# Kernel tuning notes

Hardware: AMD Instinct MI355X
Metric: run time of the kernel (lower is better)

The kernel has to match this reference:

```python
import jax, jax.numpy as jnp
import numpy as np

N, C, H, W = 4, 256, 64, 64
D = 128  # inter_channels = C // 2


def setup_inputs() -> dict:
    key = jax.random.key(0)
    ks = jax.random.split(key, 9)
    s = 0.05  # weight scale
    return {
        "x": jax.random.normal(ks[0], (N, C, H, W), jnp.float32),
        "Wg": jax.random.normal(ks[1], (D, C), jnp.float32) * s,
        "bg": jax.random.normal(ks[2], (D,), jnp.float32) * s,
        "Wt": jax.random.normal(ks[3], (D, C), jnp.float32) * s,
        "bt": jax.random.normal(ks[4], (D,), jnp.float32) * s,
        "Wp": jax.random.normal(ks[5], (D, C), jnp.float32) * s,
        "bp": jax.random.normal(ks[6], (D,), jnp.float32) * s,
        "Wz": jax.random.normal(ks[7], (C, D), jnp.float32) * s,
        "bz": jax.random.normal(ks[8], (C,), jnp.float32) * s,
    }


def reference(x, Wg, bg, Wt, bt, Wp, bp, Wz, bz):
    # NonLocalBlock, mode='embedded', dimension=2, bn_layer=False.
    # 1x1 convs are per-pixel linear maps over channels.
    n, c, h, w = x.shape
    xf = x.reshape(n, c, h * w)                                  # (N,C,S)
    g_x = jnp.einsum('dc,ncs->nds', Wg, xf) + bg[None, :, None]  # (N,D,S)
    th = jnp.einsum('dc,ncs->nds', Wt, xf) + bt[None, :, None]   # (N,D,S)
    ph = jnp.einsum('dc,ncs->nds', Wp, xf) + bp[None, :, None]   # (N,D,S)
    f = jnp.einsum('nds,ndt->nst', th, ph)                       # (N,S,S)
    att = jax.nn.softmax(f, axis=-1)
    y = jnp.einsum('nst,ndt->nds', att, g_x)                     # (N,D,S)
    w_y = jnp.einsum('cd,nds->ncs', Wz, y) + bz[None, :, None]   # (N,C,S)
    return (w_y + xf).reshape(n, c, h, w)
```

## Files before the change

### kernel.cpp

```cpp
#include <hip/hip_runtime.h>
#include <math.h>

#define N_ 4
#define C_ 256
#define D_ 128
#define S_ 4096
#define LOG2E 1.4426950408889634f
#define SPLIT 4
#define TPS 16

typedef __attribute__((ext_vector_type(4))) float f32x4;
typedef __attribute__((ext_vector_type(16))) float f32x16;
typedef __attribute__((ext_vector_type(8))) short short8;
typedef __attribute__((ext_vector_type(8))) unsigned short ushort8;
typedef __attribute__((ext_vector_type(4))) unsigned short ushort4v;

#define MFMA16(a, b, c) __builtin_amdgcn_mfma_f32_16x16x32_bf16((a), (b), (c), 0, 0, 0)
#define MFMA32(a, b, c) __builtin_amdgcn_mfma_f32_32x32x16_bf16((a), (b), (c), 0, 0, 0)

__device__ __forceinline__ unsigned short f2bf(float f) {
  union { float f; unsigned int u; } v; v.f = f;
  unsigned int r = v.u + 0x7fffu + ((v.u >> 16) & 1u);
  return (unsigned short)(r >> 16);
}
__device__ __forceinline__ float bf2f(unsigned short u) {
  union { unsigned int u; float f; } v; v.u = ((unsigned int)u) << 16;
  return v.f;
}
__device__ __forceinline__ unsigned cvtpk(float lo, float hi) {
  unsigned r;
  asm("v_cvt_pk_bf16_f32 %0, %1, %2" : "=v"(r) : "v"(lo), "v"(hi));
  return r;
}
__device__ __forceinline__ float vmax16(const f32x16& v) {
  float a = fmaxf(fmaxf(v[0], v[1]), fmaxf(v[2], v[3]));
  float b = fmaxf(fmaxf(v[4], v[5]), fmaxf(v[6], v[7]));
  float c = fmaxf(fmaxf(v[8], v[9]), fmaxf(v[10], v[11]));
  float d = fmaxf(fmaxf(v[12], v[13]), fmaxf(v[14], v[15]));
  return fmaxf(fmaxf(a, b), fmaxf(c, d));
}
__device__ __forceinline__ float vsum16(const f32x16& v) {
  float a = (v[0] + v[1]) + (v[2] + v[3]);
  float b = (v[4] + v[5]) + (v[6] + v[7]);
  float c = (v[8] + v[9]) + (v[10] + v[11]);
  float d = (v[12] + v[13]) + (v[14] + v[15]);
  return (a + b) + (c + d);
}
__device__ __forceinline__ void gload16(const void* g, void* l) {
  __builtin_amdgcn_global_load_lds((const __attribute__((address_space(1))) unsigned int*)g,
                                   (__attribute__((address_space(3))) unsigned int*)l,
                                   16, 0, 0);
}

__global__ void k_convw(const float* __restrict__ w0, const float* __restrict__ w1,
                        const float* __restrict__ w2, const float* __restrict__ w3,
                        unsigned short* __restrict__ d0, unsigned short* __restrict__ d1,
                        unsigned short* __restrict__ d2, unsigned short* __restrict__ d3) {
  int b = blockIdx.x;
  int w = b >> 4;
  int i = (b & 15) * 256 + threadIdx.x;
  const float* s = (w == 0) ? w0 : (w == 1) ? w1 : (w == 2) ? w2 : w3;
  unsigned short* d = (w == 0) ? d0 : (w == 1) ? d1 : (w == 2) ? d2 : d3;
  const float4* sp = reinterpret_cast<const float4*>(s) + (size_t)i * 2;
  float4 a = sp[0], c = sp[1];
  ushort8 o;
  o[0] = f2bf(a.x); o[1] = f2bf(a.y); o[2] = f2bf(a.z); o[3] = f2bf(a.w);
  o[4] = f2bf(c.x); o[5] = f2bf(c.y); o[6] = f2bf(c.z); o[7] = f2bf(c.w);
  reinterpret_cast<ushort8*>(d)[i] = o;
}

__global__ __launch_bounds__(256, 3) void k_proj(
    const float* __restrict__ x,
    const unsigned short* __restrict__ wg, const unsigned short* __restrict__ wt,
    const unsigned short* __restrict__ wp,
    const float* __restrict__ bg, const float* __restrict__ bt, const float* __restrict__ bp,
    unsigned short* __restrict__ qb, unsigned short* __restrict__ kb, unsigned short* __restrict__ vb)
{
  __shared__ __align__(16) unsigned short xs[C_ * 64];
  const int tid = threadIdx.x;
  const int p = blockIdx.x >> 8;
  const int n = (blockIdx.x >> 6) & 3;
  const int s0 = (blockIdx.x & 63) << 6;
  const float* xsrc = x + (size_t)n * C_ * S_ + s0;
#pragma unroll
  for (int i = 0; i < 16; ++i) {
    int ch = i * 256 + tid;
    int c = ch >> 4, s4 = (ch & 15) << 2;
    float4 v = *reinterpret_cast<const float4*>(xsrc + (size_t)c * S_ + s4);
    ushort4v o;
    o[0] = f2bf(v.x); o[1] = f2bf(v.y); o[2] = f2bf(v.z); o[3] = f2bf(v.w);
    *reinterpret_cast<ushort4v*>(xs + c * 64 + s4) = o;
  }
  __syncthreads();
  const int lane = tid & 63, wid = tid >> 6;
  const int l15 = lane & 15, g = lane >> 4;
  const int scol = wid * 16 + l15;

  short8 bx[8];
#pragma unroll
  for (int kc = 0; kc < 8; ++kc) {
    int cb = kc * 32 + g * 8;
    short8 t;
#pragma unroll
    for (int j = 0; j < 8; ++j) t[j] = (short)xs[(cb + j) * 64 + scol];
    bx[kc] = t;
  }

  const unsigned short* W = (p == 0) ? wg : ((p == 1) ? wt : wp);
  const float* bias = (p == 0) ? bg : ((p == 1) ? bt : bp);
  const f32x4 fz = {0.f, 0.f, 0.f, 0.f};
  f32x4 acc[8];
#pragma unroll
  for (int dt = 0; dt < 8; ++dt) acc[dt] = fz;
#pragma unroll
  for (int dt = 0; dt < 8; ++dt) {
    const unsigned short* wrow = W + (size_t)(dt * 16 + l15) * C_ + g * 8;
#pragma unroll
    for (int kc = 0; kc < 8; ++kc) {
      short8 a = *reinterpret_cast<const short8*>(wrow + kc * 32);
      acc[dt] = MFMA16(a, bx[kc], acc[dt]);
    }
  }
  if (p == 0) {
#pragma unroll
    for (int dt = 0; dt < 8; ++dt) {
#pragma unroll
      for (int r = 0; r < 4; ++r) {
        int d = dt * 16 + 4 * g + r;
        vb[((size_t)n * D_ + d) * S_ + s0 + scol] = f2bf(acc[dt][r] + bias[d]);
      }
    }
  } else {
    unsigned short* dst = (p == 1) ? qb : kb;
    unsigned short* row = dst + ((size_t)(n * S_) + s0 + scol) * D_;
#pragma unroll
    for (int dt = 0; dt < 8; ++dt) {
      ushort4v o;
#pragma unroll
      for (int r = 0; r < 4; ++r) o[r] = f2bf(acc[dt][r] + bias[dt * 16 + 4 * g + r]);
      *reinterpret_cast<ushort4v*>(row + dt * 16 + 4 * g) = o;
    }
  }
}

__global__ __launch_bounds__(512, 2) void k_attn(
    const unsigned short* __restrict__ qb, const unsigned short* __restrict__ kb,
    const unsigned short* __restrict__ vb,
    unsigned short* __restrict__ opart, float2* __restrict__ ml)
{
  __shared__ __align__(16) unsigned short ksm[2][64 * 128];
  __shared__ __align__(16) unsigned short vsm[2][128 * 64];
  const int tid = threadIdx.x, lane = tid & 63, w = tid >> 6;
  const int l31 = lane & 31, hi = lane >> 5;
  const int b = blockIdx.x;
  const int sp = b & 3, qt = (b >> 2) & 15, n = b >> 6;
  const int q0 = qt << 8;

  unsigned koff[2], voff[2], ubo[2];
#pragma unroll
  for (int j = 0; j < 2; ++j) {
    int f = j * 512 + tid;
    int kr = f >> 4, kc = f & 15;
    koff[j] = kr * D_ + ((kc ^ (kr & 7)) << 3);
    int vr = f >> 3, vc = f & 7;
    voff[j] = vr * S_ + ((vc ^ (vr & 7)) << 3);
    ubo[j] = (unsigned)(j * 512 + (tid & 448)) * 8;
  }
  const unsigned short* kb0 = kb + ((size_t)n * S_ + (size_t)sp * TPS * 64) * D_;
  const unsigned short* vb0 = vb + (size_t)n * D_ * S_ + sp * TPS * 64;

  auto stage = [&](int buf, int t) {
    const unsigned short* kt = kb0 + (size_t)t * 64 * D_;
    const unsigned short* vt = vb0 + t * 64;
#pragma unroll
    for (int j = 0; j < 2; ++j) gload16(kt + koff[j], &ksm[buf][ubo[j]]);
#pragma unroll
    for (int j = 0; j < 2; ++j) gload16(vt + voff[j], &vsm[buf][ubo[j]]);
  };

  stage(0, 0);

  const unsigned short* qsrc = qb + ((size_t)(n * S_) + q0 + w * 32 + l31) * D_;
  short8 qf[8];
#pragma unroll
  for (int k = 0; k < 8; ++k)
    qf[k] = *reinterpret_cast<const short8*>(qsrc + k * 16 + hi * 8);

  const f32x16 z16 = {0.f,0.f,0.f,0.f,0.f,0.f,0.f,0.f,0.f,0.f,0.f,0.f,0.f,0.f,0.f,0.f};
  f32x16 oacc[4];
#pragma unroll
  for (int db = 0; db < 4; ++db) oacc[db] = z16;
  float m_ = -3.4e38f, l_ = 0.f;

  __syncthreads();
  int cur = 0;

  for (int t = 0; t < TPS; ++t) {
    if (t + 1 < TPS) stage(cur ^ 1, t + 1);

    const unsigned short* ksb = ksm[cur];
    const unsigned short* vsb = vsm[cur];

    f32x16 pA = z16, pB = z16;
    __builtin_amdgcn_s_setprio(1);
#pragma unroll
    for (int ks = 0; ks < 8; ++ks) {
      int c = ks * 2 + hi;
      int r0 = l31, r1 = 32 + l31;
      short8 k0 = *reinterpret_cast<const short8*>(ksb + r0 * 128 + ((c ^ (r0 & 7)) << 3));
      short8 k1 = *reinterpret_cast<const short8*>(ksb + r1 * 128 + ((c ^ (r1 & 7)) << 3));
      pA = MFMA32(k0, qf[ks], pA);
      pB = MFMA32(k1, qf[ks], pB);
    }
    __builtin_amdgcn_s_setprio(0);

    float mrow = fmaxf(vmax16(pA), vmax16(pB));
    mrow = fmaxf(mrow, __shfl_xor(mrow, 32));
    if (!__all(mrow - m_ <= 8.0f)) {
      float mn = fmaxf(m_, mrow);
      float ss = exp2f((m_ - mn) * LOG2E);
      m_ = mn; l_ *= ss;
#pragma unroll
      for (int reg = 0; reg < 16; ++reg) {
        int rr = (reg & 3) + 8 * (reg >> 2) + 4 * hi;
        float sb = __shfl(ss, rr);
#pragma unroll
        for (int db = 0; db < 4; ++db) oacc[db][reg] *= sb;
      }
    }
#pragma unroll
    for (int i = 0; i < 16; ++i) pA[i] = exp2f((pA[i] - m_) * LOG2E);
#pragma unroll
    for (int i = 0; i < 16; ++i) pB[i] = exp2f((pB[i] - m_) * LOG2E);
    float rs = vsum16(pA) + vsum16(pB);
    l_ += rs + __shfl_xor(rs, 32);

    short8 pa[4];
#pragma unroll
    for (int ks = 0; ks < 4; ++ks) {
      const f32x16& p = (ks < 2) ? pA : pB;
      int ba = (ks & 1) * 8;
      unsigned ua0 = cvtpk(p[ba + 0], p[ba + 1]);
      unsigned ua1 = cvtpk(p[ba + 2], p[ba + 3]);
      unsigned ub0 = cvtpk(p[ba + 4], p[ba + 5]);
      unsigned ub1 = cvtpk(p[ba + 6], p[ba + 7]);
      unsigned x0 = (unsigned)__shfl_xor((int)(hi ? ua0 : ub0), 32);
      unsigned x1 = (unsigned)__shfl_xor((int)(hi ? ua1 : ub1), 32);
      union { unsigned u[4]; short8 s; } mm;
      mm.u[0] = hi ? x0 : ua0;  mm.u[1] = hi ? x1 : ua1;
      mm.u[2] = hi ? ub0 : x0;  mm.u[3] = hi ? ub1 : x1;
      pa[ks] = mm.s;
    }

    __builtin_amdgcn_s_setprio(1);
#pragma unroll
    for (int ks = 0; ks < 4; ++ks) {
      int c = ks * 2 + hi;
#pragma unroll
      for (int db = 0; db < 4; ++db) {
        int r = db * 32 + l31;
        short8 v = *reinterpret_cast<const short8*>(vsb + r * 64 + ((c ^ (r & 7)) << 3));
        oacc[db] = MFMA32(pa[ks], v, oacc[db]);
      }
    }
    __builtin_amdgcn_s_setprio(0);

    __syncthreads();
    cur ^= 1;
  }

  float linv = 1.f / l_;
  unsigned short* ob = opart + (((size_t)(n * SPLIT + sp)) * S_ + q0 + w * 32) * D_;
#pragma unroll
  for (int reg = 0; reg < 16; ++reg) {
    int rr = (reg & 3) + 8 * (reg >> 2) + 4 * hi;
    float li = __shfl(linv, rr);
#pragma unroll
    for (int db = 0; db < 4; ++db)
      ob[(size_t)rr * D_ + db * 32 + l31] = f2bf(oacc[db][reg] * li);
  }
  if (hi == 0) {
    ml[((size_t)(n * SPLIT + sp)) * S_ + q0 + w * 32 + l31] = make_float2(m_, l_);
  }
}

__global__ __launch_bounds__(256, 2) void k_final(
    const unsigned short* __restrict__ opart, const float2* __restrict__ ml,
    const unsigned short* __restrict__ wz, const float* __restrict__ bz,
    const float* __restrict__ x, float* __restrict__ out)
{
  __shared__ __align__(16) unsigned short ysm[32 * 128];
  __shared__ float wsm[32][4];
  const int tid = threadIdx.x, lane = tid & 63, wid = tid >> 6;
  const int l15 = lane & 15, g = lane >> 4;
  const int n = blockIdx.x >> 7, s0 = (blockIdx.x & 127) << 5;

  if (tid < 32) {
    int row = s0 + tid;
    float mv[4], lv[4];
    float M = -3.4e38f;
#pragma unroll
    for (int i = 0; i < 4; ++i) {
      float2 v = ml[(size_t)(n * 4 + i) * S_ + row];
      mv[i] = v.x; lv[i] = v.y;
      M = fmaxf(M, mv[i]);
    }
    float wsum = 0.f, wv[4];
#pragma unroll
    for (int i = 0; i < 4; ++i) { wv[i] = lv[i] * exp2f((mv[i] - M) * LOG2E); wsum += wv[i]; }
    float L = 1.f / wsum;
#pragma unroll
    for (int i = 0; i < 4; ++i) wsm[tid][i] = wv[i] * L;
  }
  __syncthreads();

#pragma unroll
  for (int i = 0; i < 2; ++i) {
    int ch = i * 256 + tid;
    int row = ch >> 4, d8 = ch & 15;
    const unsigned short* p = opart + ((size_t)(n * 4) * S_ + s0 + row) * D_ + d8 * 8;
    float acc[8] = {0.f, 0.f, 0.f, 0.f, 0.f, 0.f, 0.f, 0.f};
#pragma unroll
    for (int j = 0; j < 4; ++j) {
      ushort8 a = *reinterpret_cast<const ushort8*>(p + (size_t)j * S_ * D_);
      float wj = wsm[row][j];
#pragma unroll
      for (int e = 0; e < 8; ++e) acc[e] += bf2f(a[e]) * wj;
    }
    ushort8 o;
#pragma unroll
    for (int e = 0; e < 8; ++e) o[e] = f2bf(acc[e]);
    *reinterpret_cast<ushort8*>(ysm + row * 128 + ((d8 ^ (row & 7)) << 3)) = o;
  }
  __syncthreads();

  const int c0 = wid * 64;
  const f32x4 fz = {0.f, 0.f, 0.f, 0.f};
  f32x4 acc[4][2];
#pragma unroll
  for (int ct = 0; ct < 4; ++ct)
#pragma unroll
    for (int st = 0; st < 2; ++st) acc[ct][st] = fz;
#pragma unroll
  for (int kc = 0; kc < 4; ++kc) {
    short8 by[2];
#pragma unroll
    for (int st = 0; st < 2; ++st) {
      int r = st * 16 + l15;
      int ch = (kc * 4 + g) ^ (r & 7);
      by[st] = *reinterpret_cast<const short8*>(ysm + r * 128 + ch * 8);
    }
#pragma unroll
    for (int ct = 0; ct < 4; ++ct) {
      const short8 aw = *reinterpret_cast<const short8*>(
          wz + (size_t)(c0 + ct * 16 + l15) * D_ + kc * 32 + g * 8);
#pragma unroll
      for (int st = 0; st < 2; ++st) acc[ct][st] = MFMA16(aw, by[st], acc[ct][st]);
    }
  }
#pragma unroll
  for (int ct = 0; ct < 4; ++ct)
#pragma unroll
    for (int r = 0; r < 4; ++r) {
      int c = c0 + ct * 16 + 4 * g + r;
      float bias = bz[c];
#pragma unroll
      for (int st = 0; st < 2; ++st) {
        int s = s0 + st * 16 + l15;
        size_t idx = ((size_t)(n * C_ + c)) * S_ + s;
        out[idx] = acc[ct][st][r] + bias + x[idx];
      }
    }
}

extern "C" void kernel_launch(void* const* d_in, const int* in_sizes, int n_in,
                              void* d_out, int out_size, void* d_ws, size_t ws_size,
                              hipStream_t stream) {
  const float* x  = (const float*)d_in[0];
  const float* Wg = (const float*)d_in[1];
  const float* bg = (const float*)d_in[2];
  const float* Wt = (const float*)d_in[3];
  const float* bt = (const float*)d_in[4];
  const float* Wp = (const float*)d_in[5];
  const float* bp = (const float*)d_in[6];
  const float* Wz = (const float*)d_in[7];
  const float* bz = (const float*)d_in[8];
  float* out = (float*)d_out;
  char* ws = (char*)d_ws;
  const size_t MB = 1u << 20;
  unsigned short* qb    = (unsigned short*)(ws);
  unsigned short* kb    = (unsigned short*)(ws + 4 * MB);
  unsigned short* vb    = (unsigned short*)(ws + 8 * MB);
  unsigned short* opart = (unsigned short*)(ws + 12 * MB);
  float2*        mlbuf  = (float2*)(ws + 28 * MB);
  unsigned short* wgb   = (unsigned short*)(ws + 28 * MB + 524288);
  unsigned short* wtb   = (unsigned short*)(ws + 28 * MB + 524288 + 65536);
  unsigned short* wpb   = (unsigned short*)(ws + 28 * MB + 524288 + 131072);
  unsigned short* wzb   = (unsigned short*)(ws + 28 * MB + 524288 + 196608);

  k_convw<<<64, 256, 0, stream>>>(Wg, Wt, Wp, Wz, wgb, wtb, wpb, wzb);
  k_proj <<<768, 256, 0, stream>>>(x, wgb, wtb, wpb, bg, bt, bp, qb, kb, vb);
  k_attn <<<256, 512, 0, stream>>>(qb, kb, vb, opart, mlbuf);
  k_final<<<512, 256, 0, stream>>>(opart, mlbuf, wzb, bz, x, out);
}
```

Before: 105.3 us.

## Read K directly from global, halve attention block size, use permlane32 swap

The attention kernel no longer stages K tiles in shared memory. Each wave now loads its K fragments straight from global/L2 inside the QK loop, and only V stays double-buffered in LDS. Blocks shrink from 512 to 256 threads covering 128 queries, so the grid doubles and more blocks can be resident per CU. The P-fragment lane exchange uses v_permlane32_swap instead of shuffles plus selects. The cost is that every wave re-reads the same K rows from global memory, and the QK MFMAs now wait on global-load latency that the LDS pipeline used to hide.

```diff
diff --git a/kernel.cpp b/kernel.cpp
--- a/kernel.cpp
+++ b/kernel.cpp
@@ -143,39 +143,33 @@
   }
 }
 
-__global__ __launch_bounds__(512, 2) void k_attn(
+__global__ __launch_bounds__(256, 4) void k_attn(
     const unsigned short* __restrict__ qb, const unsigned short* __restrict__ kb,
     const unsigned short* __restrict__ vb,
     unsigned short* __restrict__ opart, float2* __restrict__ ml)
 {
-  __shared__ __align__(16) unsigned short ksm[2][64 * 128];
   __shared__ __align__(16) unsigned short vsm[2][128 * 64];
   const int tid = threadIdx.x, lane = tid & 63, w = tid >> 6;
   const int l31 = lane & 31, hi = lane >> 5;
   const int b = blockIdx.x;
-  const int sp = b & 3, qt = (b >> 2) & 15, n = b >> 6;
-  const int q0 = qt << 8;
-
-  unsigned koff[2], voff[2], ubo[2];
-#pragma unroll
-  for (int j = 0; j < 2; ++j) {
-    int f = j * 512 + tid;
-    int kr = f >> 4, kc = f & 15;
-    koff[j] = kr * D_ + ((kc ^ (kr & 7)) << 3);
+  const int sp = b & 3, qt = (b >> 2) & 31, n = b >> 7;
+  const int q0 = qt << 7;
+
+  unsigned voff[4], ubo[4];
+#pragma unroll
+  for (int j = 0; j < 4; ++j) {
+    int f = j * 256 + tid;
     int vr = f >> 3, vc = f & 7;
     voff[j] = vr * S_ + ((vc ^ (vr & 7)) << 3);
-    ubo[j] = (unsigned)(j * 512 + (tid & 448)) * 8;
+    ubo[j] = (unsigned)(j * 256 + (tid & 192)) * 8;
   }
   const unsigned short* kb0 = kb + ((size_t)n * S_ + (size_t)sp * TPS * 64) * D_;
   const unsigned short* vb0 = vb + (size_t)n * D_ * S_ + sp * TPS * 64;
 
   auto stage = [&](int buf, int t) {
-    const unsigned short* kt = kb0 + (size_t)t * 64 * D_;
     const unsigned short* vt = vb0 + t * 64;
 #pragma unroll
-    for (int j = 0; j < 2; ++j) gload16(kt + koff[j], &ksm[buf][ubo[j]]);
-#pragma unroll
-    for (int j = 0; j < 2; ++j) gload16(vt + voff[j], &vsm[buf][ubo[j]]);
+    for (int j = 0; j < 4; ++j) gload16(vt + voff[j], &vsm[buf][ubo[j]]);
   };
 
   stage(0, 0);
@@ -186,6 +180,9 @@
   for (int k = 0; k < 8; ++k)
     qf[k] = *reinterpret_cast<const short8*>(qsrc + k * 16 + hi * 8);
 
+  const unsigned short* krow0 = kb0 + (size_t)l31 * D_ + hi * 8;
+  const unsigned short* krow1 = kb0 + (size_t)(32 + l31) * D_ + hi * 8;
+
   const f32x16 z16 = {0.f,0.f,0.f,0.f,0.f,0.f,0.f,0.f,0.f,0.f,0.f,0.f,0.f,0.f,0.f,0.f};
   f32x16 oacc[4];
 #pragma unroll
@@ -198,17 +195,15 @@
   for (int t = 0; t < TPS; ++t) {
     if (t + 1 < TPS) stage(cur ^ 1, t + 1);
 
-    const unsigned short* ksb = ksm[cur];
     const unsigned short* vsb = vsm[cur];
+    const size_t kofs = (size_t)t * 64 * D_;
 
     f32x16 pA = z16, pB = z16;
     __builtin_amdgcn_s_setprio(1);
 #pragma unroll
     for (int ks = 0; ks < 8; ++ks) {
-      int c = ks * 2 + hi;
-      int r0 = l31, r1 = 32 + l31;
-      short8 k0 = *reinterpret_cast<const short8*>(ksb + r0 * 128 + ((c ^ (r0 & 7)) << 3));
-      short8 k1 = *reinterpret_cast<const short8*>(ksb + r1 * 128 + ((c ^ (r1 & 7)) << 3));
+      short8 k0 = *reinterpret_cast<const short8*>(krow0 + kofs + ks * 16);
+      short8 k1 = *reinterpret_cast<const short8*>(krow1 + kofs + ks * 16);
       pA = MFMA32(k0, qf[ks], pA);
       pB = MFMA32(k1, qf[ks], pB);
     }
@@ -240,15 +235,14 @@
     for (int ks = 0; ks < 4; ++ks) {
       const f32x16& p = (ks < 2) ? pA : pB;
       int ba = (ks & 1) * 8;
-      unsigned ua0 = cvtpk(p[ba + 0], p[ba + 1]);
-      unsigned ua1 = cvtpk(p[ba + 2], p[ba + 3]);
-      unsigned ub0 = cvtpk(p[ba + 4], p[ba + 5]);
-      unsigned ub1 = cvtpk(p[ba + 6], p[ba + 7]);
-      unsigned x0 = (unsigned)__shfl_xor((int)(hi ? ua0 : ub0), 32);
-      unsigned x1 = (unsigned)__shfl_xor((int)(hi ? ua1 : ub1), 32);
+      unsigned u0 = cvtpk(p[ba + 0], p[ba + 1]);
+      unsigned u1 = cvtpk(p[ba + 2], p[ba + 3]);
+      unsigned u2 = cvtpk(p[ba + 4], p[ba + 5]);
+      unsigned u3 = cvtpk(p[ba + 6], p[ba + 7]);
+      asm("v_permlane32_swap_b32 %0, %1" : "+v"(u0), "+v"(u2));
+      asm("v_permlane32_swap_b32 %0, %1" : "+v"(u1), "+v"(u3));
       union { unsigned u[4]; short8 s; } mm;
-      mm.u[0] = hi ? x0 : ua0;  mm.u[1] = hi ? x1 : ua1;
-      mm.u[2] = hi ? ub0 : x0;  mm.u[3] = hi ? ub1 : x1;
+      mm.u[0] = u0; mm.u[1] = u1; mm.u[2] = u2; mm.u[3] = u3;
       pa[ks] = mm.s;
     }
 
@@ -400,6 +394,6 @@
 
   k_convw<<<64, 256, 0, stream>>>(Wg, Wt, Wp, Wz, wgb, wtb, wpb, wzb);
   k_proj <<<768, 256, 0, stream>>>(x, wgb, wtb, wpb, bg, bt, bp, qb, kb, vb);
-  k_attn <<<256, 512, 0, stream>>>(qb, kb, vb, opart, mlbuf);
+  k_attn <<<512, 256, 0, stream>>>(qb, kb, vb, opart, mlbuf);
   k_final<<<512, 256, 0, stream>>>(opart, mlbuf, wzb, bz, x, out);
 }
```

Measured after the change: 216.5 us. 106% more time.
